# Optimization experiments

Hardware: AMD Instinct MI355X
Metric: run time of the kernel (lower is better)

The kernel has to match this reference:

```python
import jax, jax.numpy as jnp
import numpy as np

N = 50000
E = 800000
IN = 128
H = 256


def _sage_conv(x, src, dst, W_l, b_l, W_r, n_nodes):
    # PyG SAGEConv (aggr='mean'): out = lin_l(mean_{j in N(i)} x_j) + lin_r(x_i)
    msg = x[src]                                             # [E, d] gather
    agg = jax.ops.segment_sum(msg, dst, num_segments=n_nodes)  # [N, d]
    cnt = jax.ops.segment_sum(jnp.ones((src.shape[0],), x.dtype), dst,
                              num_segments=n_nodes)
    agg = agg / jnp.maximum(cnt, 1.0)[:, None]               # scatter-mean
    return agg @ W_l + b_l + x @ W_r


def setup_inputs() -> dict:
    key = jax.random.key(0)
    ks = jax.random.split(key, 12)
    s_in, s_h, s_h2 = 1.0 / np.sqrt(IN), 1.0 / np.sqrt(H), 1.0 / np.sqrt(H // 2)
    return {
        "x": jax.random.normal(ks[0], (N, IN), jnp.float32),
        "edge_index": jax.random.randint(ks[1], (2, E), 0, N, dtype=jnp.int32),
        # conv1: in -> H
        "W1_l": jax.random.uniform(ks[2], (IN, H), jnp.float32, -s_in, s_in),
        "b1_l": jnp.zeros((H,), jnp.float32),
        "W1_r": jax.random.uniform(ks[3], (IN, H), jnp.float32, -s_in, s_in),
        # conv2: H -> H
        "W2_l": jax.random.uniform(ks[4], (H, H), jnp.float32, -s_h, s_h),
        "b2_l": jnp.zeros((H,), jnp.float32),
        "W2_r": jax.random.uniform(ks[5], (H, H), jnp.float32, -s_h, s_h),
        # risk head: H -> H//2 -> 1
        "Wh1": jax.random.uniform(ks[6], (H, H // 2), jnp.float32, -s_h, s_h),
        "bh1": jax.random.uniform(ks[7], (H // 2,), jnp.float32, -s_h, s_h),
        "Wh2": jax.random.uniform(ks[8], (H // 2, 1), jnp.float32, -s_h2, s_h2),
        "bh2": jax.random.uniform(ks[9], (1,), jnp.float32, -s_h2, s_h2),
    }


def reference(x, edge_index, W1_l, b1_l, W1_r, W2_l, b2_l, W2_r,
              Wh1, bh1, Wh2, bh2):
    src, dst = edge_index[0], edge_index[1]
    h = jax.nn.relu(_sage_conv(x, src, dst, W1_l, b1_l, W1_r, N))
    h = jax.nn.relu(_sage_conv(h, src, dst, W2_l, b2_l, W2_r, N))
    # risk head (dropout is identity in inference)
    h = jax.nn.relu(h @ Wh1 + bh1)
    return jax.nn.sigmoid(h @ Wh2 + bh2)            # [N, 1]
```

## Files before the change

kernel.cpp:

```cpp
#include <hip/hip_runtime.h>
#include <cstdint>
#include <cstddef>

#define N_NODES 50000
#define N_PAD 50048
#define N_EDGES 800000
#define DIM_IN 128
#define DIM_H 256
#define CAP 64
#define NBKT 391
#define BCAP 2560
#define BINA_BLOCKS 400
#define EPB 2000

using u16 = unsigned short;
using u32 = unsigned int;
using u8 = unsigned char;

typedef __attribute__((ext_vector_type(8))) short bf16x8;
typedef __attribute__((ext_vector_type(4))) float f32x4;
typedef __attribute__((ext_vector_type(2))) float f32x2;

__device__ __forceinline__ u16 f2bf(float x) {
    u32 u = __float_as_uint(x);
    u32 r = (u + 0x7fffu + ((u >> 16) & 1u)) >> 16;
    return (u16)r;
}

__device__ __forceinline__ u8 enc1_sw(float f) {
    u32 u = __float_as_uint(f);
    u32 s = (u >> 24) & 0x80u;
    u32 a = u & 0x7fffffffu;
    if (a >= 0x43e00000u) return (u8)(s | 0x7e);
    if (a < 0x3c800000u) return (u8)s;
    u32 r = a + 0x7ffffu + ((a >> 20) & 1u);
    u32 e8 = (r >> 23) - 120u;
    if (e8 >= 16u) return (u8)(s | 0x7e);
    return (u8)(s | (e8 << 3) | ((r >> 20) & 7u));
}

__device__ __forceinline__ u32 enc4(float f0, float f1, float f2, float f3) {
#if __has_builtin(__builtin_amdgcn_cvt_pk_fp8_f32)
    int w = __builtin_amdgcn_cvt_pk_fp8_f32(f0, f1, 0, false);
    w = __builtin_amdgcn_cvt_pk_fp8_f32(f2, f3, w, true);
    return (u32)w;
#else
    return (u32)enc1_sw(f0) | ((u32)enc1_sw(f1) << 8) |
           ((u32)enc1_sw(f2) << 16) | ((u32)enc1_sw(f3) << 24);
#endif
}

__device__ __forceinline__ u8 enc1(float f) {
#if __has_builtin(__builtin_amdgcn_cvt_pk_fp8_f32)
    return (u8)(__builtin_amdgcn_cvt_pk_fp8_f32(f, 0.f, 0, false) & 0xff);
#else
    return enc1_sw(f);
#endif
}

__device__ __forceinline__ void dec_u32(float* o, u32 w) {
#if __has_builtin(__builtin_amdgcn_cvt_pk_f32_fp8)
    f32x2 a = __builtin_amdgcn_cvt_pk_f32_fp8(w, false);
    f32x2 b = __builtin_amdgcn_cvt_pk_f32_fp8(w, true);
    o[0] = a[0]; o[1] = a[1]; o[2] = b[0]; o[3] = b[1];
#else
    #pragma unroll
    for (int k = 0; k < 4; ++k) {
        u32 x = (w >> (8 * k)) & 0xffu;
        u32 bits = ((x & 0x80u) << 24) | ((x & 0x7fu) << 20);
        o[k] = __uint_as_float(bits) * __uint_as_float(0x7b800000u);
    }
#endif
}

__device__ __forceinline__ void gld_lds16(const u16* g, u16* l) {
    __builtin_amdgcn_global_load_lds(
        (__attribute__((address_space(1))) void*)g,
        (__attribute__((address_space(3))) void*)l, 16, 0, 0);
}

__global__ __launch_bounds__(256) void binA(
    const int* __restrict__ src, const int* __restrict__ dst,
    int* __restrict__ gcur, int2* __restrict__ binbuf) {
    __shared__ int hist[NBKT];
    __shared__ int base[NBKT];
    const int tid = threadIdx.x;
    const int e0 = blockIdx.x * EPB;
    const int e1 = min(e0 + EPB, N_EDGES);
    for (int t = tid; t < NBKT; t += 256) hist[t] = 0;
    __syncthreads();
    for (int i = e0 + tid; i < e1; i += 256)
        atomicAdd(&hist[dst[i] >> 7], 1);
    __syncthreads();
    for (int t = tid; t < NBKT; t += 256) {
        int h = hist[t];
        base[t] = h ? atomicAdd(&gcur[t], h) : 0;
    }
    __syncthreads();
    for (int t = tid; t < NBKT; t += 256) hist[t] = 0;
    __syncthreads();
    for (int i = e0 + tid; i < e1; i += 256) {
        int d = dst[i];
        int b = d >> 7;
        int o = base[b] + atomicAdd(&hist[b], 1);
        if (o < (b + 1) * BCAP) binbuf[o] = make_int2(src[i], d);
    }
}

__global__ __launch_bounds__(256) void binB(
    const int* __restrict__ gcur, const int2* __restrict__ binbuf,
    int* __restrict__ cnt, int* __restrict__ csr) {
    __shared__ int lcnt[128];
    __shared__ int lcsr[128 * CAP];
    const int b = blockIdx.x;
    const int tid = threadIdx.x;
    if (tid < 128) lcnt[tid] = 0;
    __syncthreads();
    int gc = gcur[b] - b * BCAP;
    if (gc > BCAP) gc = BCAP;
    for (int i = tid; i < gc; i += 256) {
        int2 p = binbuf[b * BCAP + i];
        int n = p.y & 127;
        int slot = atomicAdd(&lcnt[n], 1);
        if (slot < CAP) lcsr[n * CAP + slot] = p.x;
    }
    __syncthreads();
    const uint4* ls = reinterpret_cast<const uint4*>(lcsr);
    uint4* gs = reinterpret_cast<uint4*>(csr + (size_t)b * 128 * CAP);
    for (int i = tid; i < 128 * CAP / 4; i += 256) gs[i] = ls[i];
    if (tid < 128) {
        int v = b * 128 + tid;
        if (v < N_NODES) cnt[v] = lcnt[tid];
    }
}

__global__ __launch_bounds__(256) void prep(
    const float* __restrict__ x,
    const float* __restrict__ W1_l, const float* __restrict__ W1_r,
    const float* __restrict__ W2_l, const float* __restrict__ W2_r,
    const float* __restrict__ Wh1,
    u16* __restrict__ x_hi, u32* __restrict__ x_f8,
    u16* __restrict__ w1l, u16* __restrict__ w1r,
    u16* __restrict__ w2l, u16* __restrict__ w2r, u16* __restrict__ wh1,
    int* __restrict__ gcur) {
    int b = blockIdx.x, tid = threadIdx.x;
    if (b < 2) {
        int i = b * 256 + tid;
        if (i < NBKT) gcur[i] = i * BCAP;
        return;
    }
    b -= 2;
    if (b < 6250) {
        int i = b * 256 + tid;
        float4 v = reinterpret_cast<const float4*>(x)[i];
        ushort4 h;
        h.x = f2bf(v.x); h.y = f2bf(v.y); h.z = f2bf(v.z); h.w = f2bf(v.w);
        reinterpret_cast<ushort4*>(x_hi)[i] = h;
        x_f8[i] = enc4(v.x, v.y, v.z, v.w);
        return;
    }
    b -= 6250;
    if (b < 128) {
        int idx = b * 256 + tid; int m = idx >> 7, k = idx & 127;
        w1l[idx] = f2bf(W1_l[(size_t)k * 256 + m]); return;
    }
    b -= 128;
    if (b < 128) {
        int idx = b * 256 + tid; int m = idx >> 7, k = idx & 127;
        w1r[idx] = f2bf(W1_r[(size_t)k * 256 + m]); return;
    }
    b -= 128;
    if (b < 256) {
        int idx = b * 256 + tid; int m = idx >> 8, k = idx & 255;
        w2l[idx] = f2bf(W2_l[(size_t)k * 256 + m]); return;
    }
    b -= 256;
    if (b < 256) {
        int idx = b * 256 + tid; int m = idx >> 8, k = idx & 255;
        w2r[idx] = f2bf(W2_r[(size_t)k * 256 + m]); return;
    }
    b -= 256;
    {
        int idx = b * 256 + tid; int m = idx >> 8, k = idx & 255;
        wh1[idx] = f2bf(Wh1[(size_t)k * 128 + m]);
    }
}

__device__ __forceinline__ void acc16_add(float* acc, uint4 a) {
    float t[4];
    dec_u32(t, a.x); acc[0] += t[0]; acc[1] += t[1]; acc[2] += t[2]; acc[3] += t[3];
    dec_u32(t, a.y); acc[4] += t[0]; acc[5] += t[1]; acc[6] += t[2]; acc[7] += t[3];
    dec_u32(t, a.z); acc[8] += t[0]; acc[9] += t[1]; acc[10] += t[2]; acc[11] += t[3];
    dec_u32(t, a.w); acc[12] += t[0]; acc[13] += t[1]; acc[14] += t[2]; acc[15] += t[3];
}

template <int U4ROW>
__global__ __launch_bounds__(256) void aggregate_f8(
    const uint4* __restrict__ tab, const int* __restrict__ cnt,
    const int* __restrict__ csr, u16* __restrict__ out_hi, int n_nodes) {
    constexpr int EPI = 64 / U4ROW;
    constexpr int D = U4ROW * 16;
    const int lane = threadIdx.x & 63;
    const int v = blockIdx.x * 4 + (threadIdx.x >> 6);
    if (v >= n_nodes) return;
    const int q = lane & (U4ROW - 1);
    const int e = lane / U4ROW;
    const int d = cnt[v];
    const int dl = min(d, CAP);
    const int myidx = (lane < dl) ? csr[v * CAP + lane] : 0;
    float acc[16] = {};
    int j = 0;
    for (; j + 2 * EPI <= dl; j += 2 * EPI) {
        int i0 = __shfl(myidx, j + e, 64);
        int i1 = __shfl(myidx, j + EPI + e, 64);
        uint4 a = tab[(size_t)i0 * U4ROW + q];
        uint4 b = tab[(size_t)i1 * U4ROW + q];
        acc16_add(acc, a);
        acc16_add(acc, b);
    }
    for (; j + EPI <= dl; j += EPI) {
        int i0 = __shfl(myidx, j + e, 64);
        uint4 a = tab[(size_t)i0 * U4ROW + q];
        acc16_add(acc, a);
    }
    int r = dl - j;
    if (r > 0) {
        int ee = (e < r) ? e : 0;
        int i0 = __shfl(myidx, j + ee, 64);
        uint4 a = tab[(size_t)i0 * U4ROW + q];
        if (e < r) acc16_add(acc, a);
    }
    #pragma unroll
    for (int s = U4ROW; s < 64; s <<= 1)
        #pragma unroll
        for (int i = 0; i < 16; ++i) acc[i] += __shfl_xor(acc[i], s, 64);
    const float inv = 1.f / (float)((d > 0) ? d : 1);
    if (e == 0) {
        u32 w[8];
        #pragma unroll
        for (int k = 0; k < 8; ++k) {
            float m0 = acc[2 * k] * inv, m1 = acc[2 * k + 1] * inv;
            w[k] = ((u32)f2bf(m1) << 16) | f2bf(m0);
        }
        u16* dp = out_hi + (size_t)v * D + q * 16;
        *reinterpret_cast<uint4*>(dp) = *reinterpret_cast<uint4*>(&w[0]);
        *reinterpret_cast<uint4*>(dp + 8) = *reinterpret_cast<uint4*>(&w[4]);
    }
}

template <int MODE>
__global__ __launch_bounds__(512) void gemm_fused(
    const u16* __restrict__ Ah1, const u16* __restrict__ Ah2,
    const u16* __restrict__ Bh1, const u16* __restrict__ Bh2,
    const float* __restrict__ bias,
    const u16* __restrict__ wh1t, const float* __restrict__ bh1,
    const float* __restrict__ wh2, const float* __restrict__ bh2,
    u16* __restrict__ Chi, u8* __restrict__ Cf8, float* __restrict__ outF,
    int nrows, int K) {
    __shared__ __align__(16) u16 SMEM[(MODE == 1) ? 37888 : 24576];

    const int tid = threadIdx.x;
    const int lane = tid & 63;
    const int w = tid >> 6;
    const int wr = w >> 2, wc = w & 3;
    const int row0 = blockIdx.x * 128;

    f32x4 zero4 = {0.f, 0.f, 0.f, 0.f};
    f32x4 acc[4][4];
    #pragma unroll
    for (int i = 0; i < 4; ++i)
        #pragma unroll
        for (int j = 0; j < 4; ++j) acc[i][j] = zero4;

    const int srow = lane >> 2;
    const int swz = (((lane & 3) ^ (srow & 3)) * 8);

    const int nks = K >> 5;
    const int NIT = 2 * nks;

    auto stage = [&](int it, int buf) {
        const int ph = (it >= nks) ? 1 : 0;
        const int kk = it - ph * nks;
        const u16* Ab = ph ? Ah2 : Ah1;
        const u16* Bb = ph ? Bh2 : Bh1;
        u16* base = SMEM + buf * 12288;
        #pragma unroll
        for (int t = 0; t < 3; ++t) {
            int slab = w * 3 + t;
            if (slab < 8) {
                int grow = row0 + slab * 16 + srow;
                if (grow > nrows - 1) grow = nrows - 1;
                gld_lds16(Ab + (size_t)grow * K + kk * 32 + swz, base + slab * 512);
            } else {
                int gcol = (slab - 8) * 16 + srow;
                gld_lds16(Bb + (size_t)gcol * K + kk * 32 + swz,
                          base + 4096 + (slab - 8) * 512);
            }
        }
    };

    stage(0, 0);
    __syncthreads();
    int cur = 0;
    for (int it = 0; it < NIT; ++it) {
        if (it + 1 < NIT) stage(it + 1, cur ^ 1);
        const char* As_ = (const char*)(SMEM + cur * 12288);
        const char* Bs_ = As_ + 8192;
        bf16x8 af[4], bfr[4];
        #pragma unroll
        for (int i = 0; i < 4; ++i) {
            int tr = wr * 64 + i * 16 + (lane & 15);
            af[i] = *reinterpret_cast<const bf16x8*>(
                As_ + tr * 64 + (((lane >> 4) ^ (tr & 3)) * 16));
        }
        #pragma unroll
        for (int j = 0; j < 4; ++j) {
            int tc = wc * 64 + j * 16 + (lane & 15);
            bfr[j] = *reinterpret_cast<const bf16x8*>(
                Bs_ + tc * 64 + (((lane >> 4) ^ (tc & 3)) * 16));
        }
        #pragma unroll
        for (int i = 0; i < 4; ++i)
            #pragma unroll
            for (int j = 0; j < 4; ++j)
                acc[i][j] = __builtin_amdgcn_mfma_f32_16x16x32_bf16(
                    af[i], bfr[j], acc[i][j], 0, 0, 0);
        __syncthreads();
        cur ^= 1;
    }

    if (MODE == 0) {
        u16* hL = SMEM;
        u8* fL = (u8*)SMEM + 32768;
        #pragma unroll
        for (int half = 0; half < 2; ++half) {
            if (wr == half) {
                #pragma unroll
                for (int i = 0; i < 4; ++i)
                    #pragma unroll
                    for (int j = 0; j < 4; ++j) {
                        int col = wc * 64 + j * 16 + (lane & 15);
                        float b = bias[col];
                        #pragma unroll
                        for (int r = 0; r < 4; ++r) {
                            int rl = i * 16 + (lane >> 4) * 4 + r;
                            float v = fmaxf(acc[i][j][r] + b, 0.f);
                            hL[rl * 256 + col] = f2bf(v);
                            fL[rl * 256 + col] = enc1(v);
                        }
                    }
            }
            __syncthreads();
            size_t gr0 = (size_t)(row0 + half * 64);
            uint4* gh = reinterpret_cast<uint4*>(Chi + gr0 * 256);
            const uint4* lh = reinterpret_cast<const uint4*>(hL);
            #pragma unroll
            for (int k2 = 0; k2 < 4; ++k2) gh[tid + k2 * 512] = lh[tid + k2 * 512];
            uint4* gf = reinterpret_cast<uint4*>(Cf8 + gr0 * 256);
            const uint4* lf = reinterpret_cast<const uint4*>(fL);
            #pragma unroll
            for (int k2 = 0; k2 < 2; ++k2) gf[tid + k2 * 512] = lf[tid + k2 * 512];
            __syncthreads();
        }
    } else {
        u16* Bs2 = SMEM + 32768;
        float* hpart = (float*)(SMEM + 36864);
        {
            int gcol = w * 16 + srow;
            gld_lds16(wh1t + (size_t)gcol * 256 + 0 * 32 + swz, Bs2 + w * 512);
        }
        char* hb = (char*)SMEM;
        #pragma unroll
        for (int i = 0; i < 4; ++i)
            #pragma unroll
            for (int j = 0; j < 4; ++j) {
                int col = wc * 64 + j * 16 + (lane & 15);
                float b = bias[col];
                #pragma unroll
                for (int r = 0; r < 4; ++r) {
                    int row = wr * 64 + i * 16 + (lane >> 4) * 4 + r;
                    float v = fmaxf(acc[i][j][r] + b, 0.f);
                    int byt = row * 512 + col * 2;
                    *(u16*)(hb + (byt ^ ((row & 7) << 4))) = f2bf(v);
                }
            }
        __syncthreads();

        const int whr = wr, whc = wc;
        f32x4 acc2[4][2];
        #pragma unroll
        for (int i = 0; i < 4; ++i) { acc2[i][0] = zero4; acc2[i][1] = zero4; }
        for (int kk = 0; kk < 8; ++kk) {
            const char* B2 = (const char*)Bs2;
            bf16x8 af2[4], bfr2[2];
            #pragma unroll
            for (int i = 0; i < 4; ++i) {
                int row = whr * 64 + i * 16 + (lane & 15);
                int byt = row * 512 + kk * 64 + (lane >> 4) * 16;
                af2[i] = *reinterpret_cast<const bf16x8*>(hb + (byt ^ ((row & 7) << 4)));
            }
            #pragma unroll
            for (int j = 0; j < 2; ++j) {
                int tc = whc * 32 + j * 16 + (lane & 15);
                bfr2[j] = *reinterpret_cast<const bf16x8*>(
                    B2 + tc * 64 + (((lane >> 4) ^ (tc & 3)) * 16));
            }
            __syncthreads();
            if (kk + 1 < 8) {
                int gcol = w * 16 + srow;
                gld_lds16(wh1t + (size_t)gcol * 256 + (kk + 1) * 32 + swz,
                          Bs2 + w * 512);
            }
            #pragma unroll
            for (int i = 0; i < 4; ++i)
                #pragma unroll
                for (int j = 0; j < 2; ++j)
                    acc2[i][j] = __builtin_amdgcn_mfma_f32_16x16x32_bf16(
                        af2[i], bfr2[j], acc2[i][j], 0, 0, 0);
            __syncthreads();
        }

        float pr[4][4];
        #pragma unroll
        for (int i = 0; i < 4; ++i)
            #pragma unroll
            for (int r = 0; r < 4; ++r) pr[i][r] = 0.f;
        #pragma unroll
        for (int j = 0; j < 2; ++j) {
            int col = whc * 32 + j * 16 + (lane & 15);
            float b1 = bh1[col];
            float wv = wh2[col];
            #pragma unroll
            for (int i = 0; i < 4; ++i)
                #pragma unroll
                for (int r = 0; r < 4; ++r)
                    pr[i][r] += fmaxf(acc2[i][j][r] + b1, 0.f) * wv;
        }
        #pragma unroll
        for (int i = 0; i < 4; ++i)
            #pragma unroll
            for (int r = 0; r < 4; ++r) {
                float s = pr[i][r];
                s += __shfl_xor(s, 1, 64);
                s += __shfl_xor(s, 2, 64);
                s += __shfl_xor(s, 4, 64);
                s += __shfl_xor(s, 8, 64);
                pr[i][r] = s;
            }
        if ((lane & 15) == 0) {
            #pragma unroll
            for (int i = 0; i < 4; ++i)
                #pragma unroll
                for (int r = 0; r < 4; ++r)
                    hpart[whc * 128 + whr * 64 + i * 16 + (lane >> 4) * 4 + r] = pr[i][r];
        }
        __syncthreads();
        if (tid < 128) {
            int row = row0 + tid;
            if (row < nrows) {
                float s = hpart[tid] + hpart[128 + tid] + hpart[256 + tid]
                        + hpart[384 + tid] + bh2[0];
                outF[row] = 1.f / (1.f + expf(-s));
            }
        }
    }
}

static inline size_t align256(size_t x) { return (x + 255) & ~(size_t)255; }

extern "C" void kernel_launch(void* const* d_in, const int* in_sizes, int n_in,
                              void* d_out, int out_size, void* d_ws, size_t ws_size,
                              hipStream_t stream) {
    const float* x    = (const float*)d_in[0];
    const int* ei     = (const int*)d_in[1];
    const float* W1_l = (const float*)d_in[2];
    const float* b1_l = (const float*)d_in[3];
    const float* W1_r = (const float*)d_in[4];
    const float* W2_l = (const float*)d_in[5];
    const float* b2_l = (const float*)d_in[6];
    const float* W2_r = (const float*)d_in[7];
    const float* Wh1  = (const float*)d_in[8];
    const float* bh1  = (const float*)d_in[9];
    const float* Wh2  = (const float*)d_in[10];
    const float* bh2  = (const float*)d_in[11];
    float* out = (float*)d_out;

    const int* src = ei;
    const int* dst = ei + N_EDGES;

    const size_t SZ_N128 = (size_t)N_NODES * DIM_IN * sizeof(u16);
    const size_t SZ_W128x256 = (size_t)128 * 256 * sizeof(u16);

    char* ws = (char*)d_ws;
    size_t off_ = 0;
    auto alloc = [&](size_t bytes) { size_t o = off_; off_ += align256(bytes); return o; };

    size_t o_cnt = alloc((size_t)N_PAD * 4);
    size_t o_gcur = alloc((size_t)512 * 4);
    size_t o_csr = alloc((size_t)N_PAD * CAP * 4);
    size_t o_bin = alloc((size_t)NBKT * BCAP * 8);
    size_t o_w1l = alloc(SZ_W128x256);
    size_t o_w1r = alloc(SZ_W128x256);
    size_t o_w2l = alloc(2 * SZ_W128x256);
    size_t o_w2r = alloc(2 * SZ_W128x256);
    size_t o_wh1 = alloc(SZ_W128x256);
    size_t o_xh  = alloc(SZ_N128);
    size_t o_xf8 = alloc((size_t)N_NODES * DIM_IN);
    size_t o_a1  = alloc(SZ_N128);
    size_t o_h1  = alloc((size_t)N_PAD * DIM_H * sizeof(u16));
    size_t o_h1f = alloc((size_t)N_PAD * DIM_H);
    size_t o_a2  = alloc((size_t)N_NODES * DIM_H * sizeof(u16));
    if (ws_size < off_) return;

    int* cnt  = (int*)(ws + o_cnt);
    int* gcur = (int*)(ws + o_gcur);
    int* csr  = (int*)(ws + o_csr);
    int2* binbuf = (int2*)(ws + o_bin);
    u16* w1l_h = (u16*)(ws + o_w1l);
    u16* w1r_h = (u16*)(ws + o_w1r);
    u16* w2l_h = (u16*)(ws + o_w2l);
    u16* w2r_h = (u16*)(ws + o_w2r);
    u16* wh1_h = (u16*)(ws + o_wh1);
    u16* x_hi    = (u16*)(ws + o_xh);
    u32* x_f8    = (u32*)(ws + o_xf8);
    u16* agg1_hi = (u16*)(ws + o_a1);
    u16* h1_hi   = (u16*)(ws + o_h1);
    u8*  h1_f8   = (u8*)(ws + o_h1f);
    u16* agg2_hi = (u16*)(ws + o_a2);

    prep<<<2 + 6250 + 128 + 128 + 256 + 256 + 128, 256, 0, stream>>>(
        x, W1_l, W1_r, W2_l, W2_r, Wh1,
        x_hi, x_f8, w1l_h, w1r_h, w2l_h, w2r_h, wh1_h, gcur);

    binA<<<BINA_BLOCKS, 256, 0, stream>>>(src, dst, gcur, binbuf);
    binB<<<NBKT, 256, 0, stream>>>(gcur, binbuf, cnt, csr);

    const int RB = (N_NODES + 127) / 128;
    const int AB = (N_NODES + 3) / 4;

    aggregate_f8<8><<<AB, 256, 0, stream>>>(
        (const uint4*)x_f8, cnt, csr, agg1_hi, N_NODES);
    gemm_fused<0><<<RB, 512, 0, stream>>>(
        agg1_hi, x_hi, w1l_h, w1r_h, b1_l,
        nullptr, nullptr, nullptr, nullptr, h1_hi, h1_f8, nullptr, N_NODES, 128);

    aggregate_f8<16><<<AB, 256, 0, stream>>>(
        (const uint4*)h1_f8, cnt, csr, agg2_hi, N_NODES);
    gemm_fused<1><<<RB, 512, 0, stream>>>(
        agg2_hi, h1_hi, w2l_h, w2r_h, b2_l,
        wh1_h, bh1, Wh2, bh2, nullptr, nullptr, out, N_NODES, 256);
}
```

Before: 146.9 us.

## Fuse neighbor mean aggregation into GEMM prologue via LDS tile

```diff
diff --git a/kernel.cpp b/kernel.cpp
--- a/kernel.cpp
+++ b/kernel.cpp
@@ -77,6 +77,14 @@
     __builtin_amdgcn_global_load_lds(
         (__attribute__((address_space(1))) void*)g,
         (__attribute__((address_space(3))) void*)l, 16, 0, 0);
+}
+
+__device__ __forceinline__ void acc16_add(float* acc, uint4 a) {
+    float t[4];
+    dec_u32(t, a.x); acc[0] += t[0]; acc[1] += t[1]; acc[2] += t[2]; acc[3] += t[3];
+    dec_u32(t, a.y); acc[4] += t[0]; acc[5] += t[1]; acc[6] += t[2]; acc[7] += t[3];
+    dec_u32(t, a.z); acc[8] += t[0]; acc[9] += t[1]; acc[10] += t[2]; acc[11] += t[3];
+    dec_u32(t, a.w); acc[12] += t[0]; acc[13] += t[1]; acc[14] += t[2]; acc[15] += t[3];
 }
 
 __global__ __launch_bounds__(256) void binA(
@@ -186,199 +194,206 @@
     }
 }
 
-__device__ __forceinline__ void acc16_add(float* acc, uint4 a) {
-    float t[4];
-    dec_u32(t, a.x); acc[0] += t[0]; acc[1] += t[1]; acc[2] += t[2]; acc[3] += t[3];
-    dec_u32(t, a.y); acc[4] += t[0]; acc[5] += t[1]; acc[6] += t[2]; acc[7] += t[3];
-    dec_u32(t, a.z); acc[8] += t[0]; acc[9] += t[1]; acc[10] += t[2]; acc[11] += t[3];
-    dec_u32(t, a.w); acc[12] += t[0]; acc[13] += t[1]; acc[14] += t[2]; acc[15] += t[3];
-}
-
-template <int U4ROW>
-__global__ __launch_bounds__(256) void aggregate_f8(
-    const uint4* __restrict__ tab, const int* __restrict__ cnt,
-    const int* __restrict__ csr, u16* __restrict__ out_hi, int n_nodes) {
-    constexpr int EPI = 64 / U4ROW;
-    constexpr int D = U4ROW * 16;
-    const int lane = threadIdx.x & 63;
-    const int v = blockIdx.x * 4 + (threadIdx.x >> 6);
-    if (v >= n_nodes) return;
-    const int q = lane & (U4ROW - 1);
-    const int e = lane / U4ROW;
-    const int d = cnt[v];
-    const int dl = min(d, CAP);
-    const int myidx = (lane < dl) ? csr[v * CAP + lane] : 0;
-    float acc[16] = {};
-    int j = 0;
-    for (; j + 2 * EPI <= dl; j += 2 * EPI) {
-        int i0 = __shfl(myidx, j + e, 64);
-        int i1 = __shfl(myidx, j + EPI + e, 64);
-        uint4 a = tab[(size_t)i0 * U4ROW + q];
-        uint4 b = tab[(size_t)i1 * U4ROW + q];
-        acc16_add(acc, a);
-        acc16_add(acc, b);
-    }
-    for (; j + EPI <= dl; j += EPI) {
-        int i0 = __shfl(myidx, j + e, 64);
-        uint4 a = tab[(size_t)i0 * U4ROW + q];
-        acc16_add(acc, a);
-    }
-    int r = dl - j;
-    if (r > 0) {
-        int ee = (e < r) ? e : 0;
-        int i0 = __shfl(myidx, j + ee, 64);
-        uint4 a = tab[(size_t)i0 * U4ROW + q];
-        if (e < r) acc16_add(acc, a);
-    }
-    #pragma unroll
-    for (int s = U4ROW; s < 64; s <<= 1)
-        #pragma unroll
-        for (int i = 0; i < 16; ++i) acc[i] += __shfl_xor(acc[i], s, 64);
-    const float inv = 1.f / (float)((d > 0) ? d : 1);
-    if (e == 0) {
-        u32 w[8];
-        #pragma unroll
-        for (int k = 0; k < 8; ++k) {
-            float m0 = acc[2 * k] * inv, m1 = acc[2 * k + 1] * inv;
-            w[k] = ((u32)f2bf(m1) << 16) | f2bf(m0);
-        }
-        u16* dp = out_hi + (size_t)v * D + q * 16;
-        *reinterpret_cast<uint4*>(dp) = *reinterpret_cast<uint4*>(&w[0]);
-        *reinterpret_cast<uint4*>(dp + 8) = *reinterpret_cast<uint4*>(&w[4]);
-    }
-}
-
 template <int MODE>
 __global__ __launch_bounds__(512) void gemm_fused(
-    const u16* __restrict__ Ah1, const u16* __restrict__ Ah2,
-    const u16* __restrict__ Bh1, const u16* __restrict__ Bh2,
-    const float* __restrict__ bias,
+    const uint4* __restrict__ tab, const int* __restrict__ cnt,
+    const int* __restrict__ csr,
+    const u16* __restrict__ A2, const u16* __restrict__ B0,
+    const u16* __restrict__ B1, const float* __restrict__ bias,
     const u16* __restrict__ wh1t, const float* __restrict__ bh1,
     const float* __restrict__ wh2, const float* __restrict__ bh2,
     u16* __restrict__ Chi, u8* __restrict__ Cf8, float* __restrict__ outF,
-    int nrows, int K) {
-    __shared__ __align__(16) u16 SMEM[(MODE == 1) ? 37888 : 24576];
+    int nrows) {
+    constexpr int KD = MODE ? 256 : 128;
+    constexpr int U4R = KD / 16;
+    constexpr int EPI = 64 / U4R;
+    constexpr int nks = KD / 32;
+    constexpr int NIT = 2 * nks;
+    constexpr int AGG_OFF = 40960;
+    __shared__ __align__(16) u16 SMEM[(40960 + 64 * KD * 2) / 2];
 
     const int tid = threadIdx.x;
     const int lane = tid & 63;
     const int w = tid >> 6;
     const int wr = w >> 2, wc = w & 3;
-    const int row0 = blockIdx.x * 128;
-
-    f32x4 zero4 = {0.f, 0.f, 0.f, 0.f};
-    f32x4 acc[4][4];
-    #pragma unroll
-    for (int i = 0; i < 4; ++i)
-        #pragma unroll
-        for (int j = 0; j < 4; ++j) acc[i][j] = zero4;
+    const int row0 = blockIdx.x * 64;
 
     const int srow = lane >> 2;
     const int swz = (((lane & 3) ^ (srow & 3)) * 8);
 
-    const int nks = K >> 5;
-    const int NIT = 2 * nks;
+    {
+        const int q = lane & (U4R - 1);
+        const int e = lane / U4R;
+        char* aggb = (char*)SMEM + AGG_OFF;
+        for (int n = 0; n < 8; ++n) {
+            int lrow = w * 8 + n;
+            int v = row0 + lrow;
+            int d = (v < N_NODES) ? cnt[v] : 0;
+            int dl = min(d, CAP);
+            int myidx = (lane < dl) ? csr[v * CAP + lane] : 0;
+            float acc[16] = {};
+            int j = 0;
+            for (; j + 2 * EPI <= dl; j += 2 * EPI) {
+                int i0 = __shfl(myidx, j + e, 64);
+                int i1 = __shfl(myidx, j + EPI + e, 64);
+                uint4 a = tab[(size_t)i0 * U4R + q];
+                uint4 b = tab[(size_t)i1 * U4R + q];
+                acc16_add(acc, a);
+                acc16_add(acc, b);
+            }
+            for (; j + EPI <= dl; j += EPI) {
+                int i0 = __shfl(myidx, j + e, 64);
+                uint4 a = tab[(size_t)i0 * U4R + q];
+                acc16_add(acc, a);
+            }
+            int r = dl - j;
+            if (r > 0) {
+                int ee = (e < r) ? e : 0;
+                int i0 = __shfl(myidx, j + ee, 64);
+                uint4 a = tab[(size_t)i0 * U4R + q];
+                if (e < r) acc16_add(acc, a);
+            }
+            #pragma unroll
+            for (int s = U4R; s < 64; s <<= 1)
+                #pragma unroll
+                for (int i = 0; i < 16; ++i) acc[i] += __shfl_xor(acc[i], s, 64);
+            const float inv = 1.f / (float)((d > 0) ? d : 1);
+            if (e == 0) {
+                u32 wd[8];
+                #pragma unroll
+                for (int k = 0; k < 8; ++k) {
+                    float m0 = acc[2 * k] * inv, m1 = acc[2 * k + 1] * inv;
+                    wd[k] = ((u32)f2bf(m1) << 16) | f2bf(m0);
+                }
+                char* rowp = aggb + (size_t)lrow * (KD * 2);
+                int sw = (lrow & 7) << 4;
+                *(uint4*)(rowp + ((q * 32) ^ sw)) = *(uint4*)&wd[0];
+                *(uint4*)(rowp + ((q * 32 + 16) ^ sw)) = *(uint4*)&wd[4];
+            }
+        }
+    }
+
+    f32x4 zero4 = {0.f, 0.f, 0.f, 0.f};
+    f32x4 acc[2][4];
+    #pragma unroll
+    for (int i = 0; i < 2; ++i)
+        #pragma unroll
+        for (int j = 0; j < 4; ++j) acc[i][j] = zero4;
 
     auto stage = [&](int it, int buf) {
         const int ph = (it >= nks) ? 1 : 0;
         const int kk = it - ph * nks;
-        const u16* Ab = ph ? Ah2 : Ah1;
-        const u16* Bb = ph ? Bh2 : Bh1;
-        u16* base = SMEM + buf * 12288;
-        #pragma unroll
-        for (int t = 0; t < 3; ++t) {
-            int slab = w * 3 + t;
-            if (slab < 8) {
-                int grow = row0 + slab * 16 + srow;
-                if (grow > nrows - 1) grow = nrows - 1;
-                gld_lds16(Ab + (size_t)grow * K + kk * 32 + swz, base + slab * 512);
-            } else {
-                int gcol = (slab - 8) * 16 + srow;
-                gld_lds16(Bb + (size_t)gcol * K + kk * 32 + swz,
-                          base + 4096 + (slab - 8) * 512);
+        char* base = (char*)SMEM + buf * 20480;
+        if (ph == 0) {
+            #pragma unroll
+            for (int t = 0; t < 2; ++t) {
+                int s = w * 2 + t;
+                int gcol = s * 16 + srow;
+                gld_lds16(B0 + (size_t)gcol * KD + kk * 32 + swz,
+                          (u16*)(base + 4096 + s * 1024));
+            }
+        } else {
+            #pragma unroll
+            for (int t = 0; t < 3; ++t) {
+                int s = w * 3 + t;
+                if (s >= 20) continue;
+                if (s < 4) {
+                    int grow = row0 + s * 16 + srow;
+                    if (grow > nrows - 1) grow = nrows - 1;
+                    gld_lds16(A2 + (size_t)grow * KD + kk * 32 + swz,
+                              (u16*)(base + s * 1024));
+                } else {
+                    int gcol = (s - 4) * 16 + srow;
+                    gld_lds16(B1 + (size_t)gcol * KD + kk * 32 + swz,
+                              (u16*)(base + 4096 + (s - 4) * 1024));
+                }
             }
         }
     };
 
     stage(0, 0);
     __syncthreads();
-    int cur = 0;
     for (int it = 0; it < NIT; ++it) {
-        if (it + 1 < NIT) stage(it + 1, cur ^ 1);
-        const char* As_ = (const char*)(SMEM + cur * 12288);
-        const char* Bs_ = As_ + 8192;
-        bf16x8 af[4], bfr[4];
-        #pragma unroll
-        for (int i = 0; i < 4; ++i) {
-            int tr = wr * 64 + i * 16 + (lane & 15);
-            af[i] = *reinterpret_cast<const bf16x8*>(
-                As_ + tr * 64 + (((lane >> 4) ^ (tr & 3)) * 16));
+        if (it + 1 < NIT) stage(it + 1, (it + 1) & 1);
+        const int ph = (it >= nks) ? 1 : 0;
+        const char* base_ = (const char*)SMEM + (it & 1) * 20480;
+        bf16x8 af[2], bfr[4];
+        if (ph == 0) {
+            const char* aggb = (const char*)SMEM + AGG_OFF;
+            const int kit = it;
+            #pragma unroll
+            for (int i = 0; i < 2; ++i) {
+                int tr = wr * 32 + i * 16 + (lane & 15);
+                af[i] = *reinterpret_cast<const bf16x8*>(
+                    aggb + (size_t)tr * (KD * 2) +
+                    ((kit * 64 + (lane >> 4) * 16) ^ ((tr & 7) << 4)));
+            }
+        } else {
+            #pragma unroll
+            for (int i = 0; i < 2; ++i) {
+                int tr = wr * 32 + i * 16 + (lane & 15);
+                af[i] = *reinterpret_cast<const bf16x8*>(
+                    base_ + tr * 64 + (((lane >> 4) ^ (tr & 3)) * 16));
+            }
         }
         #pragma unroll
         for (int j = 0; j < 4; ++j) {
             int tc = wc * 64 + j * 16 + (lane & 15);
             bfr[j] = *reinterpret_cast<const bf16x8*>(
-                Bs_ + tc * 64 + (((lane >> 4) ^ (tc & 3)) * 16));
-        }
-        #pragma unroll
-        for (int i = 0; i < 4; ++i)
+                base_ + 4096 + tc * 64 + (((lane >> 4) ^ (tc & 3)) * 16));
+        }
+        #pragma unroll
+        for (int i = 0; i < 2; ++i)
             #pragma unroll
             for (int j = 0; j < 4; ++j)
                 acc[i][j] = __builtin_amdgcn_mfma_f32_16x16x32_bf16(
                     af[i], bfr[j], acc[i][j], 0, 0, 0);
         __syncthreads();
-        cur ^= 1;
     }
 
     if (MODE == 0) {
         u16* hL = SMEM;
         u8* fL = (u8*)SMEM + 32768;
         #pragma unroll
-        for (int half = 0; half < 2; ++half) {
-            if (wr == half) {
-                #pragma unroll
-                for (int i = 0; i < 4; ++i)
-                    #pragma unroll
-                    for (int j = 0; j < 4; ++j) {
-                        int col = wc * 64 + j * 16 + (lane & 15);
-                        float b = bias[col];
-                        #pragma unroll
-                        for (int r = 0; r < 4; ++r) {
-                            int rl = i * 16 + (lane >> 4) * 4 + r;
-                            float v = fmaxf(acc[i][j][r] + b, 0.f);
-                            hL[rl * 256 + col] = f2bf(v);
-                            fL[rl * 256 + col] = enc1(v);
-                        }
-                    }
-            }
-            __syncthreads();
-            size_t gr0 = (size_t)(row0 + half * 64);
-            uint4* gh = reinterpret_cast<uint4*>(Chi + gr0 * 256);
-            const uint4* lh = reinterpret_cast<const uint4*>(hL);
-            #pragma unroll
-            for (int k2 = 0; k2 < 4; ++k2) gh[tid + k2 * 512] = lh[tid + k2 * 512];
-            uint4* gf = reinterpret_cast<uint4*>(Cf8 + gr0 * 256);
-            const uint4* lf = reinterpret_cast<const uint4*>(fL);
-            #pragma unroll
-            for (int k2 = 0; k2 < 2; ++k2) gf[tid + k2 * 512] = lf[tid + k2 * 512];
-            __syncthreads();
-        }
+        for (int i = 0; i < 2; ++i)
+            #pragma unroll
+            for (int j = 0; j < 4; ++j) {
+                int col = wc * 64 + j * 16 + (lane & 15);
+                float b = bias[col];
+                #pragma unroll
+                for (int r = 0; r < 4; ++r) {
+                    int row = wr * 32 + i * 16 + (lane >> 4) * 4 + r;
+                    float v = fmaxf(acc[i][j][r] + b, 0.f);
+                    hL[row * 256 + col] = f2bf(v);
+                    fL[row * 256 + col] = enc1(v);
+                }
+            }
+        __syncthreads();
+        uint4* gh = reinterpret_cast<uint4*>(Chi + (size_t)row0 * 256);
+        const uint4* lh = reinterpret_cast<const uint4*>(hL);
+        #pragma unroll
+        for (int k2 = 0; k2 < 4; ++k2) gh[tid + k2 * 512] = lh[tid + k2 * 512];
+        uint4* gf = reinterpret_cast<uint4*>(Cf8 + (size_t)row0 * 256);
+        const uint4* lf = reinterpret_cast<const uint4*>(fL);
+        #pragma unroll
+        for (int k2 = 0; k2 < 2; ++k2) gf[tid + k2 * 512] = lf[tid + k2 * 512];
     } else {
-        u16* Bs2 = SMEM + 32768;
-        float* hpart = (float*)(SMEM + 36864);
+        u16* Bs2 = SMEM + 16384;
+        float* hpart = (float*)((char*)SMEM + AGG_OFF);
         {
             int gcol = w * 16 + srow;
             gld_lds16(wh1t + (size_t)gcol * 256 + 0 * 32 + swz, Bs2 + w * 512);
         }
         char* hb = (char*)SMEM;
         #pragma unroll
-        for (int i = 0; i < 4; ++i)
+        for (int i = 0; i < 2; ++i)
             #pragma unroll
             for (int j = 0; j < 4; ++j) {
                 int col = wc * 64 + j * 16 + (lane & 15);
                 float b = bias[col];
                 #pragma unroll
                 for (int r = 0; r < 4; ++r) {
-                    int row = wr * 64 + i * 16 + (lane >> 4) * 4 + r;
+                    int row = wr * 32 + i * 16 + (lane >> 4) * 4 + r;
                     float v = fmaxf(acc[i][j][r] + b, 0.f);
                     int byt = row * 512 + col * 2;
                     *(u16*)(hb + (byt ^ ((row & 7) << 4))) = f2bf(v);
@@ -386,22 +401,21 @@
             }
         __syncthreads();
 
-        const int whr = wr, whc = wc;
-        f32x4 acc2[4][2];
-        #pragma unroll
-        for (int i = 0; i < 4; ++i) { acc2[i][0] = zero4; acc2[i][1] = zero4; }
+        f32x4 acc2[2][2];
+        #pragma unroll
+        for (int i = 0; i < 2; ++i) { acc2[i][0] = zero4; acc2[i][1] = zero4; }
         for (int kk = 0; kk < 8; ++kk) {
             const char* B2 = (const char*)Bs2;
-            bf16x8 af2[4], bfr2[2];
-            #pragma unroll
-            for (int i = 0; i < 4; ++i) {
-                int row = whr * 64 + i * 16 + (lane & 15);
+            bf16x8 af2[2], bfr2[2];
+            #pragma unroll
+            for (int i = 0; i < 2; ++i) {
+                int row = wr * 32 + i * 16 + (lane & 15);
                 int byt = row * 512 + kk * 64 + (lane >> 4) * 16;
                 af2[i] = *reinterpret_cast<const bf16x8*>(hb + (byt ^ ((row & 7) << 4)));
             }
             #pragma unroll
             for (int j = 0; j < 2; ++j) {
-                int tc = whc * 32 + j * 16 + (lane & 15);
+                int tc = wc * 32 + j * 16 + (lane & 15);
                 bfr2[j] = *reinterpret_cast<const bf16x8*>(
                     B2 + tc * 64 + (((lane >> 4) ^ (tc & 3)) * 16));
             }
@@ -412,7 +426,7 @@
                           Bs2 + w * 512);
             }
             #pragma unroll
-            for (int i = 0; i < 4; ++i)
+            for (int i = 0; i < 2; ++i)
                 #pragma unroll
                 for (int j = 0; j < 2; ++j)
                     acc2[i][j] = __builtin_amdgcn_mfma_f32_16x16x32_bf16(
@@ -420,24 +434,24 @@
             __syncthreads();
         }
 
-        float pr[4][4];
-        #pragma unroll
-        for (int i = 0; i < 4; ++i)
+        float pr[2][4];
+        #pragma unroll
+        for (int i = 0; i < 2; ++i)
             #pragma unroll
             for (int r = 0; r < 4; ++r) pr[i][r] = 0.f;
         #pragma unroll
         for (int j = 0; j < 2; ++j) {
-            int col = whc * 32 + j * 16 + (lane & 15);
+            int col = wc * 32 + j * 16 + (lane & 15);
             float b1 = bh1[col];
             float wv = wh2[col];
             #pragma unroll
-            for (int i = 0; i < 4; ++i)
+            for (int i = 0; i < 2; ++i)
                 #pragma unroll
                 for (int r = 0; r < 4; ++r)
                     pr[i][r] += fmaxf(acc2[i][j][r] + b1, 0.f) * wv;
         }
         #pragma unroll
-        for (int i = 0; i < 4; ++i)
+        for (int i = 0; i < 2; ++i)
             #pragma unroll
             for (int r = 0; r < 4; ++r) {
                 float s = pr[i][r];
@@ -449,17 +463,17 @@
             }
         if ((lane & 15) == 0) {
             #pragma unroll
-            for (int i = 0; i < 4; ++i)
+            for (int i = 0; i < 2; ++i)
                 #pragma unroll
                 for (int r = 0; r < 4; ++r)
-                    hpart[whc * 128 + whr * 64 + i * 16 + (lane >> 4) * 4 + r] = pr[i][r];
+                    hpart[wc * 64 + wr * 32 + i * 16 + (lane >> 4) * 4 + r] = pr[i][r];
         }
         __syncthreads();
-        if (tid < 128) {
+        if (tid < 64) {
             int row = row0 + tid;
             if (row < nrows) {
-                float s = hpart[tid] + hpart[128 + tid] + hpart[256 + tid]
-                        + hpart[384 + tid] + bh2[0];
+                float s = hpart[tid] + hpart[64 + tid] + hpart[128 + tid]
+                        + hpart[192 + tid] + bh2[0];
                 outF[row] = 1.f / (1.f + expf(-s));
             }
         }
@@ -506,10 +520,8 @@
     size_t o_wh1 = alloc(SZ_W128x256);
     size_t o_xh  = alloc(SZ_N128);
     size_t o_xf8 = alloc((size_t)N_NODES * DIM_IN);
-    size_t o_a1  = alloc(SZ_N128);
     size_t o_h1  = alloc((size_t)N_PAD * DIM_H * sizeof(u16));
     size_t o_h1f = alloc((size_t)N_PAD * DIM_H);
-    size_t o_a2  = alloc((size_t)N_NODES * DIM_H * sizeof(u16));
     if (ws_size < off_) return;
 
     int* cnt  = (int*)(ws + o_cnt);
@@ -523,10 +535,8 @@
     u16* wh1_h = (u16*)(ws + o_wh1);
     u16* x_hi    = (u16*)(ws + o_xh);
     u32* x_f8    = (u32*)(ws + o_xf8);
-    u16* agg1_hi = (u16*)(ws + o_a1);
     u16* h1_hi   = (u16*)(ws + o_h1);
     u8*  h1_f8   = (u8*)(ws + o_h1f);
-    u16* agg2_hi = (u16*)(ws + o_a2);
 
     prep<<<2 + 6250 + 128 + 128 + 256 + 256 + 128, 256, 0, stream>>>(
         x, W1_l, W1_r, W2_l, W2_r, Wh1,
@@ -535,18 +545,13 @@
     binA<<<BINA_BLOCKS, 256, 0, stream>>>(src, dst, gcur, binbuf);
     binB<<<NBKT, 256, 0, stream>>>(gcur, binbuf, cnt, csr);
 
-    const int RB = (N_NODES + 127) / 128;
-    const int AB = (N_NODES + 3) / 4;
-
-    aggregate_f8<8><<<AB, 256, 0, stream>>>(
-        (const uint4*)x_f8, cnt, csr, agg1_hi, N_NODES);
+    const int RB = N_PAD / 64;
+
     gemm_fused<0><<<RB, 512, 0, stream>>>(
-        agg1_hi, x_hi, w1l_h, w1r_h, b1_l,
-        nullptr, nullptr, nullptr, nullptr, h1_hi, h1_f8, nullptr, N_NODES, 128);
-
-    aggregate_f8<16><<<AB, 256, 0, stream>>>(
-        (const uint4*)h1_f8, cnt, csr, agg2_hi, N_NODES);
+        (const uint4*)x_f8, cnt, csr, x_hi, w1l_h, w1r_h, b1_l,
+        nullptr, nullptr, nullptr, nullptr, h1_hi, h1_f8, nullptr, N_NODES);
+
     gemm_fused<1><<<RB, 512, 0, stream>>>(
-        agg2_hi, h1_hi, w2l_h, w2r_h, b2_l,
-        wh1_h, bh1, Wh2, bh2, nullptr, nullptr, out, N_NODES, 256);
-}
+        (const uint4*)h1_f8, cnt, csr, h1_hi, w2l_h, w2r_h, b2_l,
+        wh1_h, bh1, Wh2, bh2, nullptr, nullptr, out, N_NODES);
+}
```

Result: slower. 182.7 us (+24.4%).
